# Performance work log

Hardware: AMD Instinct MI355X
Metric: run time of the kernel (lower is better)

Reference implementation:

```python
import jax, jax.numpy as jnp
import numpy as np

D_MODEL = 1024
NUM_HEADS = 16
HEAD_DIM = D_MODEL // NUM_HEADS


def setup_inputs() -> dict:
    key = jax.random.key(0)
    ks = jax.random.split(key, 9)
    B, S = 4, 2048
    s = 1.0 / np.sqrt(D_MODEL)
    return {
        "x": jax.random.normal(ks[0], (B, S, D_MODEL), dtype=jnp.float32),
        "Wq": jax.random.normal(ks[1], (D_MODEL, D_MODEL), dtype=jnp.float32) * s,
        "bq": jnp.zeros((D_MODEL,), dtype=jnp.float32),
        "Wk": jax.random.normal(ks[2], (D_MODEL, HEAD_DIM), dtype=jnp.float32) * s,
        "bk": jnp.zeros((HEAD_DIM,), dtype=jnp.float32),
        "Wv": jax.random.normal(ks[3], (D_MODEL, HEAD_DIM), dtype=jnp.float32) * s,
        "bv": jnp.zeros((HEAD_DIM,), dtype=jnp.float32),
        "Wo": jax.random.normal(ks[4], (D_MODEL, D_MODEL), dtype=jnp.float32) * s,
        "bo": jnp.zeros((D_MODEL,), dtype=jnp.float32),
    }


def reference(x, Wq, bq, Wk, bk, Wv, bv, Wo, bo):
    B, S, _ = x.shape
    H, Dh = NUM_HEADS, HEAD_DIM
    # projections
    Q = (x @ Wq + bq).reshape(B, S, H, Dh).transpose(0, 2, 1, 3)  # [B,H,S,Dh]
    K = x @ Wk + bk  # [B,S,Dh] (single shared KV head)
    V = x @ Wv + bv  # [B,S,Dh]
    # scores: Q @ K^T, broadcasting the single K head over all query heads
    A = jnp.einsum("bhqd,bkd->bhqk", Q, K)  # [B,H,S,S]
    causal = jnp.tril(jnp.ones((S, S), dtype=bool))
    A = jnp.where(causal, A, -jnp.inf)
    # original divides AFTER masking; -inf stays -inf so math is identical
    P = jax.nn.softmax(A / np.sqrt(Dh).astype(np.float32), axis=-1)
    O = jnp.einsum("bhqk,bkd->bhqd", P, V)  # [B,H,S,Dh]
    O = O.transpose(0, 2, 1, 3).reshape(B, S, H * Dh)
    return O @ Wo + bo
```

## Files before the change

### kernel.cpp

```cpp
#include <hip/hip_runtime.h>
#include <hip/hip_bf16.h>

typedef __bf16 bf16_t;
typedef __bf16 bf16x4 __attribute__((ext_vector_type(4)));
typedef __bf16 bf16x8 __attribute__((ext_vector_type(8)));
typedef float f32x4 __attribute__((ext_vector_type(4)));

#define AS1(p) ((const __attribute__((address_space(1))) void*)(p))
#define AS3(p) ((__attribute__((address_space(3))) void*)(p))

__device__ __forceinline__ f32x4 mfma16(bf16x8 a, bf16x8 b, f32x4 c) {
  return __builtin_amdgcn_mfma_f32_16x16x32_bf16(a, b, c, 0, 0, 0);
}

__global__ void prep(const float* __restrict__ x, const float* __restrict__ Wq,
                     const float* __restrict__ Wk, const float* __restrict__ Wv,
                     const float* __restrict__ Wo, const float* __restrict__ bk,
                     const float* __restrict__ bv, bf16_t* __restrict__ xb,
                     bf16_t* __restrict__ WqT, bf16_t* __restrict__ WkvT,
                     bf16_t* __restrict__ WoT, float* __restrict__ bkv) {
  const int u = blockIdx.x;
  if (u >= 545) {
    int i = ((u - 545) * 256 + threadIdx.x) * 4;
    float4 v = *(const float4*)(x + i);
    bf16x4 o = {(bf16_t)v.x, (bf16_t)v.y, (bf16_t)v.z, (bf16_t)v.w};
    *(bf16x4*)(xb + i) = o;
    return;
  }
  if (u == 544) {
    if (threadIdx.x < 128)
      bkv[threadIdx.x] = (threadIdx.x < 64) ? bk[threadIdx.x] : bv[threadIdx.x - 64];
    return;
  }
  const float* W; bf16_t* Wt; int N, bx, by;
  if (u < 256)      { W = Wq; Wt = WqT;             N = 1024; bx = u & 15;        by = u >> 4; }
  else if (u < 272) { W = Wk; Wt = WkvT;            N = 64;   bx = 0;             by = u - 256; }
  else if (u < 288) { W = Wv; Wt = WkvT + 64 * 1024; N = 64;  bx = 0;             by = u - 272; }
  else              { W = Wo; Wt = WoT;             N = 1024; bx = (u - 288) & 15; by = (u - 288) >> 4; }
  __shared__ float t[64][65];
  const int n0 = bx * 64, k0 = by * 64;
  const int tx = threadIdx.x & 63, ty = threadIdx.x >> 6;
#pragma unroll
  for (int i = 0; i < 16; ++i)
    t[ty * 16 + i][tx] = W[(size_t)(k0 + ty * 16 + i) * N + n0 + tx];
  __syncthreads();
#pragma unroll
  for (int i = 0; i < 16; ++i)
    Wt[(size_t)(n0 + ty * 16 + i) * 1024 + k0 + tx] = (bf16_t)t[tx][ty * 16 + i];
}

__global__ __launch_bounds__(256, 2)
void gemm_nt_bias_b16(const bf16_t* __restrict__ A, const bf16_t* __restrict__ Bt,
                      const float* __restrict__ bias, bf16_t* __restrict__ C,
                      int M, int N, int K) {
  __shared__ __align__(16) bf16_t As[128 * 32];
  __shared__ __align__(16) bf16_t Bs[128 * 32];
  const int tid = threadIdx.x;
  const int w = tid >> 6, l = tid & 63;
  const int l15 = l & 15, q = l >> 4;
  const int m0 = blockIdx.x * 128, n0 = blockIdx.y * 128;
  const int mw = (w >> 1) * 64, nw = (w & 1) * 64;
  f32x4 acc[4][4] = {};
  const int kb = (l & 3) * 8;
  int rA[2], rB[2];
#pragma unroll
  for (int i = 0; i < 2; ++i) {
    int row = (i * 4 + w) * 16 + (l >> 2);
    rA[i] = m0 + row;
    int rb = n0 + row; if (rb >= N) rb = N - 1;
    rB[i] = rb;
  }
  for (int k0 = 0; k0 < K; k0 += 32) {
#pragma unroll
    for (int i = 0; i < 2; ++i) {
      int sg = i * 4 + w;
      __builtin_amdgcn_global_load_lds(AS1(A + (size_t)rA[i] * K + k0 + kb),
                                       AS3(As + sg * 512), 16, 0, 0);
      __builtin_amdgcn_global_load_lds(AS1(Bt + (size_t)rB[i] * K + k0 + kb),
                                       AS3(Bs + sg * 512), 16, 0, 0);
    }
    __syncthreads();
    bf16x8 af[4], bfr[4];
#pragma unroll
    for (int mi = 0; mi < 4; ++mi)
      af[mi] = *(const bf16x8*)(As + (mw + mi * 16 + l15) * 32 + q * 8);
#pragma unroll
    for (int ni = 0; ni < 4; ++ni)
      bfr[ni] = *(const bf16x8*)(Bs + (nw + ni * 16 + l15) * 32 + q * 8);
#pragma unroll
    for (int mi = 0; mi < 4; ++mi)
#pragma unroll
      for (int ni = 0; ni < 4; ++ni)
        acc[mi][ni] = mfma16(af[mi], bfr[ni], acc[mi][ni]);
    __syncthreads();
  }
#pragma unroll
  for (int ni = 0; ni < 4; ++ni) {
    int col = n0 + nw + ni * 16 + l15;
    if (col >= N) continue;
    float bv = bias[col];
#pragma unroll
    for (int mi = 0; mi < 4; ++mi)
#pragma unroll
      for (int r = 0; r < 4; ++r) {
        int row = m0 + mw + mi * 16 + q * 4 + r;
        C[(size_t)row * N + col] = (bf16_t)(acc[mi][ni][r] + bv);
      }
  }
}

__global__ __launch_bounds__(256, 2)
void gemm_kv(const bf16_t* __restrict__ A, const bf16_t* __restrict__ Bt,
             const float* __restrict__ bias, bf16_t* __restrict__ C,
             bf16_t* __restrict__ VtG, int M, int K) {
  __shared__ __align__(16) bf16_t As[128 * 32];
  __shared__ __align__(16) bf16_t Bs[128 * 32];
  const int tid = threadIdx.x;
  const int w = tid >> 6, l = tid & 63;
  const int l15 = l & 15, q = l >> 4;
  const int m0 = blockIdx.x * 128;
  const int mw = (w >> 1) * 64, nw = (w & 1) * 64;
  f32x4 acc[4][4] = {};
  const int kb = (l & 3) * 8;
  int rA[2], rB[2];
#pragma unroll
  for (int i = 0; i < 2; ++i) {
    int row = (i * 4 + w) * 16 + (l >> 2);
    rA[i] = m0 + row;
    rB[i] = row;
  }
  for (int k0 = 0; k0 < K; k0 += 32) {
#pragma unroll
    for (int i = 0; i < 2; ++i) {
      int sg = i * 4 + w;
      __builtin_amdgcn_global_load_lds(AS1(A + (size_t)rA[i] * K + k0 + kb),
                                       AS3(As + sg * 512), 16, 0, 0);
      __builtin_amdgcn_global_load_lds(AS1(Bt + (size_t)rB[i] * K + k0 + kb),
                                       AS3(Bs + sg * 512), 16, 0, 0);
    }
    __syncthreads();
    bf16x8 af[4], bfr[4];
#pragma unroll
    for (int mi = 0; mi < 4; ++mi)
      af[mi] = *(const bf16x8*)(As + (mw + mi * 16 + l15) * 32 + q * 8);
#pragma unroll
    for (int ni = 0; ni < 4; ++ni)
      bfr[ni] = *(const bf16x8*)(Bs + (nw + ni * 16 + l15) * 32 + q * 8);
#pragma unroll
    for (int mi = 0; mi < 4; ++mi)
#pragma unroll
      for (int ni = 0; ni < 4; ++ni)
        acc[mi][ni] = mfma16(af[mi], bfr[ni], acc[mi][ni]);
    __syncthreads();
  }
#pragma unroll
  for (int ni = 0; ni < 4; ++ni) {
    int col = nw + ni * 16 + l15;
    float bv = bias[col];
#pragma unroll
    for (int mi = 0; mi < 4; ++mi)
#pragma unroll
      for (int r = 0; r < 4; ++r) {
        int row = m0 + mw + mi * 16 + q * 4 + r;
        bf16_t v = (bf16_t)(acc[mi][ni][r] + bv);
        C[(size_t)row * 128 + col] = v;
        if (col >= 64)
          VtG[(size_t)((row >> 11) * 64 + (col - 64)) * 2048 + (row & 2047)] = v;
      }
  }
}

__global__ __launch_bounds__(256, 2)
void gemm_nt_bias_f32(const bf16_t* __restrict__ A, const bf16_t* __restrict__ Bt,
                      const float* __restrict__ bias, float* __restrict__ C,
                      int M, int N, int K) {
  __shared__ __align__(16) bf16_t As[128 * 32];
  __shared__ __align__(16) bf16_t Bs[128 * 32];
  const int tid = threadIdx.x;
  const int w = tid >> 6, l = tid & 63;
  const int l15 = l & 15, q = l >> 4;
  const int m0 = blockIdx.x * 128, n0 = blockIdx.y * 128;
  const int mw = (w >> 1) * 64, nw = (w & 1) * 64;
  f32x4 acc[4][4] = {};
  const int kb = (l & 3) * 8;
  int rA[2], rB[2];
#pragma unroll
  for (int i = 0; i < 2; ++i) {
    int row = (i * 4 + w) * 16 + (l >> 2);
    rA[i] = m0 + row;
    int rb = n0 + row; if (rb >= N) rb = N - 1;
    rB[i] = rb;
  }
  for (int k0 = 0; k0 < K; k0 += 32) {
#pragma unroll
    for (int i = 0; i < 2; ++i) {
      int sg = i * 4 + w;
      __builtin_amdgcn_global_load_lds(AS1(A + (size_t)rA[i] * K + k0 + kb),
                                       AS3(As + sg * 512), 16, 0, 0);
      __builtin_amdgcn_global_load_lds(AS1(Bt + (size_t)rB[i] * K + k0 + kb),
                                       AS3(Bs + sg * 512), 16, 0, 0);
    }
    __syncthreads();
    bf16x8 af[4], bfr[4];
#pragma unroll
    for (int mi = 0; mi < 4; ++mi)
      af[mi] = *(const bf16x8*)(As + (mw + mi * 16 + l15) * 32 + q * 8);
#pragma unroll
    for (int ni = 0; ni < 4; ++ni)
      bfr[ni] = *(const bf16x8*)(Bs + (nw + ni * 16 + l15) * 32 + q * 8);
#pragma unroll
    for (int mi = 0; mi < 4; ++mi)
#pragma unroll
      for (int ni = 0; ni < 4; ++ni)
        acc[mi][ni] = mfma16(af[mi], bfr[ni], acc[mi][ni]);
    __syncthreads();
  }
#pragma unroll
  for (int ni = 0; ni < 4; ++ni) {
    int col = n0 + nw + ni * 16 + l15;
    if (col >= N) continue;
    float bv = bias[col];
#pragma unroll
    for (int mi = 0; mi < 4; ++mi)
#pragma unroll
      for (int r = 0; r < 4; ++r) {
        int row = m0 + mw + mi * 16 + q * 4 + r;
        C[(size_t)row * N + col] = acc[mi][ni][r] + bv;
      }
  }
}

__device__ __forceinline__ void load_q(const bf16_t* __restrict__ Qb, int b, int h,
                                       int qt, int l15, int q,
                                       bf16x8 (&qf0)[4], bf16x8 (&qf1)[4]) {
#pragma unroll
  for (int nq = 0; nq < 4; ++nq) {
    const bf16_t* qp = Qb + (size_t)(b * 2048 + qt * 64 + nq * 16 + l15) * 1024 + h * 64 + q * 8;
    qf0[nq] = *(const bf16x8*)qp;
    qf1[nq] = *(const bf16x8*)(qp + 32);
  }
}

template <bool DIAG>
__device__ __forceinline__ void attn_step(
    const bf16_t* __restrict__ kbase, const bf16_t* __restrict__ vbase, int kt,
    int l15, int q, bf16_t* __restrict__ ps,
    const bf16x8 (&qf0)[4], const bf16x8 (&qf1)[4],
    f32x4 (&o)[4][4], float (&rs)[4]) {
  const float c1 = 0.18033688f;
  const bf16_t* kb = kbase + (size_t)kt * 64 * 128;
  bf16x8 ka0[4], ka1[4];
#pragma unroll
  for (int mk = 0; mk < 4; ++mk) {
    const bf16_t* kr = kb + (mk * 16 + l15) * 128;
    ka0[mk] = *(const bf16x8*)(kr + q * 8);
    ka1[mk] = *(const bf16x8*)(kr + 32 + q * 8);
  }
  bf16x8 va0[4], va1[4];
#pragma unroll
  for (int md = 0; md < 4; ++md) {
    const bf16_t* vr = vbase + (size_t)(md * 16 + l15) * 2048 + kt * 64;
    va0[md] = *(const bf16x8*)(vr + q * 8);
    va1[md] = *(const bf16x8*)(vr + 32 + q * 8);
  }
#pragma unroll
  for (int mh = 0; mh < 2; ++mh) {
    f32x4 s2[2][4];
    __builtin_amdgcn_s_setprio(1);
#pragma unroll
    for (int mk2 = 0; mk2 < 2; ++mk2)
#pragma unroll
      for (int nq = 0; nq < 4; ++nq) {
        f32x4 t = {0.f, 0.f, 0.f, 0.f};
        t = mfma16(ka0[mh * 2 + mk2], qf0[nq], t);
        t = mfma16(ka1[mh * 2 + mk2], qf1[nq], t);
        s2[mk2][nq] = t;
      }
    __builtin_amdgcn_s_setprio(0);
#pragma unroll
    for (int nq = 0; nq < 4; ++nq)
#pragma unroll
      for (int mk2 = 0; mk2 < 2; ++mk2) {
        const int mk = mh * 2 + mk2;
        bf16x4 pk;
#pragma unroll
        for (int r = 0; r < 4; ++r) {
          float pv = __builtin_amdgcn_exp2f(s2[mk2][nq][r] * c1 - 16.0f);
          if (DIAG && (mk * 16 + q * 4 + r) > (nq * 16 + l15)) pv = 0.f;
          rs[nq] += pv;
          pk[r] = (bf16_t)pv;
        }
        *(bf16x4*)(ps + nq * 1152 + l15 * 72 + mk * 16 + q * 4) = pk;
      }
  }
#pragma unroll
  for (int nq = 0; nq < 4; ++nq) {
    bf16x8 pb0 = *(const bf16x8*)(ps + nq * 1152 + l15 * 72 + q * 8);
    bf16x8 pb1 = *(const bf16x8*)(ps + nq * 1152 + l15 * 72 + 32 + q * 8);
    __builtin_amdgcn_s_setprio(1);
#pragma unroll
    for (int md = 0; md < 4; ++md) {
      o[md][nq] = mfma16(va0[md], pb0, o[md][nq]);
      o[md][nq] = mfma16(va1[md], pb1, o[md][nq]);
    }
    __builtin_amdgcn_s_setprio(0);
  }
}

__device__ __forceinline__ void attn_finalize(bf16_t* __restrict__ AO, int b, int h,
                                              int qt, int l15, int q,
                                              f32x4 (&o)[4][4], float (&rs)[4]) {
#pragma unroll
  for (int nq = 0; nq < 4; ++nq) {
    rs[nq] += __shfl_xor(rs[nq], 16);
    rs[nq] += __shfl_xor(rs[nq], 32);
  }
  float inv[4];
#pragma unroll
  for (int nq = 0; nq < 4; ++nq) inv[nq] = 1.f / rs[nq];
#pragma unroll
  for (int md = 0; md < 4; ++md)
#pragma unroll
    for (int nq = 0; nq < 4; ++nq) {
      bf16x4 ov = {(bf16_t)(o[md][nq][0] * inv[nq]), (bf16_t)(o[md][nq][1] * inv[nq]),
                   (bf16_t)(o[md][nq][2] * inv[nq]), (bf16_t)(o[md][nq][3] * inv[nq])};
      *(bf16x4*)(AO + (size_t)(b * 2048 + qt * 64 + nq * 16 + l15) * 1024 +
                 h * 64 + md * 16 + q * 4) = ov;
    }
}

__global__ __launch_bounds__(128, 2)
void mqa_attn9(const bf16_t* __restrict__ Qb, const bf16_t* __restrict__ KVb,
               const bf16_t* __restrict__ VtG, bf16_t* __restrict__ AO) {
  __shared__ __align__(16) bf16_t Ps[2][4][16 * 72];
  __shared__ __align__(16) float Oc[4096];
  __shared__ float RSc[256];
  const int u = blockIdx.x;
  const int b = u & 3;
  const int h = (u >> 2) & 15;
  const int p = (u >> 6) & 15;
  const int w = threadIdx.x >> 6, l = threadIdx.x & 63;
  const int l15 = l & 15, q = l >> 4;
  const int qt_h = 31 - p;
  bf16_t* ps = &Ps[w][0][0];
  const bf16_t* kbase = KVb + (size_t)b * 2048 * 128;
  const bf16_t* vbase = VtG + (size_t)b * 64 * 2048;

  bf16x8 qf0[4], qf1[4];
  f32x4 o[4][4] = {};
  float rs[4] = {0.f, 0.f, 0.f, 0.f};

  if (w == 0) {
    load_q(Qb, b, h, qt_h, l15, q, qf0, qf1);
    const int e = (p == 15) ? 16 : 17;
    for (int kt = 0; kt < e; ++kt)
      attn_step<false>(kbase, vbase, kt, l15, q, ps, qf0, qf1, o, rs);
    if (p == 15)
      attn_step<true>(kbase, vbase, 16, l15, q, ps, qf0, qf1, o, rs);
    __syncthreads();
#pragma unroll
    for (int md = 0; md < 4; ++md)
#pragma unroll
      for (int nq = 0; nq < 4; ++nq)
        o[md][nq] += *(const f32x4*)&Oc[((md * 4 + nq) * 64 + l) * 4];
#pragma unroll
    for (int nq = 0; nq < 4; ++nq) rs[nq] += RSc[l * 4 + nq];
    attn_finalize(AO, b, h, qt_h, l15, q, o, rs);
  } else {
    load_q(Qb, b, h, p, l15, q, qf0, qf1);
    for (int kt = 0; kt < p; ++kt)
      attn_step<false>(kbase, vbase, kt, l15, q, ps, qf0, qf1, o, rs);
    attn_step<true>(kbase, vbase, p, l15, q, ps, qf0, qf1, o, rs);
    attn_finalize(AO, b, h, p, l15, q, o, rs);
#pragma unroll
    for (int md = 0; md < 4; ++md)
#pragma unroll
      for (int nq = 0; nq < 4; ++nq) o[md][nq] = f32x4{0.f, 0.f, 0.f, 0.f};
    rs[0] = rs[1] = rs[2] = rs[3] = 0.f;
    if (p < 15) {
      load_q(Qb, b, h, qt_h, l15, q, qf0, qf1);
      for (int kt = 17; kt < 31 - p; ++kt)
        attn_step<false>(kbase, vbase, kt, l15, q, ps, qf0, qf1, o, rs);
      attn_step<true>(kbase, vbase, 31 - p, l15, q, ps, qf0, qf1, o, rs);
    }
#pragma unroll
    for (int md = 0; md < 4; ++md)
#pragma unroll
      for (int nq = 0; nq < 4; ++nq)
        *(f32x4*)&Oc[((md * 4 + nq) * 64 + l) * 4] = o[md][nq];
#pragma unroll
    for (int nq = 0; nq < 4; ++nq) RSc[l * 4 + nq] = rs[nq];
    __syncthreads();
  }
}

extern "C" void kernel_launch(void* const* d_in, const int* in_sizes, int n_in,
                              void* d_out, int out_size, void* d_ws, size_t ws_size,
                              hipStream_t stream) {
  (void)in_sizes; (void)n_in; (void)out_size; (void)ws_size;
  const int BS = 8192;
  const float* x  = (const float*)d_in[0];
  const float* Wq = (const float*)d_in[1];
  const float* bq = (const float*)d_in[2];
  const float* Wk = (const float*)d_in[3];
  const float* bk = (const float*)d_in[4];
  const float* Wv = (const float*)d_in[5];
  const float* bv = (const float*)d_in[6];
  const float* Wo = (const float*)d_in[7];
  const float* bo = (const float*)d_in[8];
  float* out = (float*)d_out;

  bf16_t* p = (bf16_t*)d_ws;
  bf16_t* WqT  = p; p += 1024 * 1024;
  bf16_t* WkvT = p; p += 128 * 1024;
  bf16_t* WoT  = p; p += 1024 * 1024;
  bf16_t* xb   = p; p += (size_t)BS * 1024;
  bf16_t* Qb   = p; p += (size_t)BS * 1024;
  bf16_t* KVb  = p; p += (size_t)BS * 128;
  float*  bkv  = (float*)p; p += 256;
  bf16_t* AO  = xb;
  bf16_t* VtG = WqT;

  prep<<<dim3(545 + BS * 1024 / 1024), 256, 0, stream>>>(
      x, Wq, Wk, Wv, Wo, bk, bv, xb, WqT, WkvT, WoT, bkv);

  gemm_nt_bias_b16<<<dim3(BS / 128, 8), 256, 0, stream>>>(xb, WqT, bq, Qb, BS, 1024, 1024);
  gemm_kv<<<dim3(BS / 128, 1), 256, 0, stream>>>(xb, WkvT, bkv, KVb, VtG, BS, 1024);

  mqa_attn9<<<dim3(1024), 128, 0, stream>>>(Qb, KVb, VtG, AO);

  gemm_nt_bias_f32<<<dim3(BS / 128, 8), 256, 0, stream>>>(AO, WoT, bo, out, BS, 1024, 1024);
}
```

Before: 247.9 us.

## Fuse Q and KV projection GEMMs and double-buffer K tiles in attention

Merges the Q projection GEMM and the KV projection GEMM into one launch over a 9-column-tile grid. It relies on WqT and WkvT being contiguous in the workspace (1152 rows total), with the biases concatenated into one buffer. VtG now gets its own workspace region because WqT can no longer be overwritten. The attention kernel adds a software-pipelined loop that prefetches the next K tile and the current V tile into registers before computing each step. Together these aim to remove a launch and its tail inefficiency and to hide global load latency, at the cost of higher register pressure.

```diff
diff --git a/kernel.cpp b/kernel.cpp
--- a/kernel.cpp
+++ b/kernel.cpp
@@ -15,28 +15,35 @@
 
 __global__ void prep(const float* __restrict__ x, const float* __restrict__ Wq,
                      const float* __restrict__ Wk, const float* __restrict__ Wv,
-                     const float* __restrict__ Wo, const float* __restrict__ bk,
-                     const float* __restrict__ bv, bf16_t* __restrict__ xb,
-                     bf16_t* __restrict__ WqT, bf16_t* __restrict__ WkvT,
-                     bf16_t* __restrict__ WoT, float* __restrict__ bkv) {
+                     const float* __restrict__ Wo, const float* __restrict__ bq,
+                     const float* __restrict__ bk, const float* __restrict__ bv,
+                     bf16_t* __restrict__ xb, bf16_t* __restrict__ WqT,
+                     bf16_t* __restrict__ WkvT, bf16_t* __restrict__ WoT,
+                     float* __restrict__ bqkv) {
   const int u = blockIdx.x;
-  if (u >= 545) {
-    int i = ((u - 545) * 256 + threadIdx.x) * 4;
+  if (u >= 546) {
+    int i = ((u - 546) * 256 + threadIdx.x) * 4;
     float4 v = *(const float4*)(x + i);
     bf16x4 o = {(bf16_t)v.x, (bf16_t)v.y, (bf16_t)v.z, (bf16_t)v.w};
     *(bf16x4*)(xb + i) = o;
     return;
   }
   if (u == 544) {
+    int i = threadIdx.x * 4;
+    *(float4*)(bqkv + i) = *(const float4*)(bq + i);
+    return;
+  }
+  if (u == 545) {
     if (threadIdx.x < 128)
-      bkv[threadIdx.x] = (threadIdx.x < 64) ? bk[threadIdx.x] : bv[threadIdx.x - 64];
+      bqkv[1024 + threadIdx.x] =
+          (threadIdx.x < 64) ? bk[threadIdx.x] : bv[threadIdx.x - 64];
     return;
   }
   const float* W; bf16_t* Wt; int N, bx, by;
-  if (u < 256)      { W = Wq; Wt = WqT;             N = 1024; bx = u & 15;        by = u >> 4; }
-  else if (u < 272) { W = Wk; Wt = WkvT;            N = 64;   bx = 0;             by = u - 256; }
-  else if (u < 288) { W = Wv; Wt = WkvT + 64 * 1024; N = 64;  bx = 0;             by = u - 272; }
-  else              { W = Wo; Wt = WoT;             N = 1024; bx = (u - 288) & 15; by = (u - 288) >> 4; }
+  if (u < 256)      { W = Wq; Wt = WqT;              N = 1024; bx = u & 15;         by = u >> 4; }
+  else if (u < 272) { W = Wk; Wt = WkvT;             N = 64;   bx = 0;              by = u - 256; }
+  else if (u < 288) { W = Wv; Wt = WkvT + 64 * 1024; N = 64;   bx = 0;              by = u - 272; }
+  else              { W = Wo; Wt = WoT;              N = 1024; bx = (u - 288) & 15; by = (u - 288) >> 4; }
   __shared__ float t[64][65];
   const int n0 = bx * 64, k0 = by * 64;
   const int tx = threadIdx.x & 63, ty = threadIdx.x >> 6;
@@ -50,9 +57,9 @@
 }
 
 __global__ __launch_bounds__(256, 2)
-void gemm_nt_bias_b16(const bf16_t* __restrict__ A, const bf16_t* __restrict__ Bt,
-                      const float* __restrict__ bias, bf16_t* __restrict__ C,
-                      int M, int N, int K) {
+void gemm_qkv(const bf16_t* __restrict__ A, const bf16_t* __restrict__ Bt,
+              const float* __restrict__ bias, bf16_t* __restrict__ Qb,
+              bf16_t* __restrict__ KVb, bf16_t* __restrict__ VtG, int M, int K) {
   __shared__ __align__(16) bf16_t As[128 * 32];
   __shared__ __align__(16) bf16_t Bs[128 * 32];
   const int tid = threadIdx.x;
@@ -67,8 +74,7 @@
   for (int i = 0; i < 2; ++i) {
     int row = (i * 4 + w) * 16 + (l >> 2);
     rA[i] = m0 + row;
-    int rb = n0 + row; if (rb >= N) rb = N - 1;
-    rB[i] = rb;
+    rB[i] = n0 + row;
   }
   for (int k0 = 0; k0 < K; k0 += 32) {
 #pragma unroll
@@ -97,65 +103,6 @@
 #pragma unroll
   for (int ni = 0; ni < 4; ++ni) {
     int col = n0 + nw + ni * 16 + l15;
-    if (col >= N) continue;
-    float bv = bias[col];
-#pragma unroll
-    for (int mi = 0; mi < 4; ++mi)
-#pragma unroll
-      for (int r = 0; r < 4; ++r) {
-        int row = m0 + mw + mi * 16 + q * 4 + r;
-        C[(size_t)row * N + col] = (bf16_t)(acc[mi][ni][r] + bv);
-      }
-  }
-}
-
-__global__ __launch_bounds__(256, 2)
-void gemm_kv(const bf16_t* __restrict__ A, const bf16_t* __restrict__ Bt,
-             const float* __restrict__ bias, bf16_t* __restrict__ C,
-             bf16_t* __restrict__ VtG, int M, int K) {
-  __shared__ __align__(16) bf16_t As[128 * 32];
-  __shared__ __align__(16) bf16_t Bs[128 * 32];
-  const int tid = threadIdx.x;
-  const int w = tid >> 6, l = tid & 63;
-  const int l15 = l & 15, q = l >> 4;
-  const int m0 = blockIdx.x * 128;
-  const int mw = (w >> 1) * 64, nw = (w & 1) * 64;
-  f32x4 acc[4][4] = {};
-  const int kb = (l & 3) * 8;
-  int rA[2], rB[2];
-#pragma unroll
-  for (int i = 0; i < 2; ++i) {
-    int row = (i * 4 + w) * 16 + (l >> 2);
-    rA[i] = m0 + row;
-    rB[i] = row;
-  }
-  for (int k0 = 0; k0 < K; k0 += 32) {
-#pragma unroll
-    for (int i = 0; i < 2; ++i) {
-      int sg = i * 4 + w;
-      __builtin_amdgcn_global_load_lds(AS1(A + (size_t)rA[i] * K + k0 + kb),
-                                       AS3(As + sg * 512), 16, 0, 0);
-      __builtin_amdgcn_global_load_lds(AS1(Bt + (size_t)rB[i] * K + k0 + kb),
-                                       AS3(Bs + sg * 512), 16, 0, 0);
-    }
-    __syncthreads();
-    bf16x8 af[4], bfr[4];
-#pragma unroll
-    for (int mi = 0; mi < 4; ++mi)
-      af[mi] = *(const bf16x8*)(As + (mw + mi * 16 + l15) * 32 + q * 8);
-#pragma unroll
-    for (int ni = 0; ni < 4; ++ni)
-      bfr[ni] = *(const bf16x8*)(Bs + (nw + ni * 16 + l15) * 32 + q * 8);
-#pragma unroll
-    for (int mi = 0; mi < 4; ++mi)
-#pragma unroll
-      for (int ni = 0; ni < 4; ++ni)
-        acc[mi][ni] = mfma16(af[mi], bfr[ni], acc[mi][ni]);
-    __syncthreads();
-  }
-#pragma unroll
-  for (int ni = 0; ni < 4; ++ni) {
-    int col = nw + ni * 16 + l15;
     float bv = bias[col];
 #pragma unroll
     for (int mi = 0; mi < 4; ++mi)
@@ -163,9 +110,14 @@
       for (int r = 0; r < 4; ++r) {
         int row = m0 + mw + mi * 16 + q * 4 + r;
         bf16_t v = (bf16_t)(acc[mi][ni][r] + bv);
-        C[(size_t)row * 128 + col] = v;
-        if (col >= 64)
-          VtG[(size_t)((row >> 11) * 64 + (col - 64)) * 2048 + (row & 2047)] = v;
+        if (col < 1024) {
+          Qb[(size_t)row * 1024 + col] = v;
+        } else {
+          int c2 = col - 1024;
+          KVb[(size_t)row * 128 + c2] = v;
+          if (c2 >= 64)
+            VtG[(size_t)((row >> 11) * 64 + (c2 - 64)) * 2048 + (row & 2047)] = v;
+        }
       }
   }
 }
@@ -230,39 +182,35 @@
   }
 }
 
-__device__ __forceinline__ void load_q(const bf16_t* __restrict__ Qb, int b, int h,
-                                       int qt, int l15, int q,
-                                       bf16x8 (&qf0)[4], bf16x8 (&qf1)[4]) {
-#pragma unroll
-  for (int nq = 0; nq < 4; ++nq) {
-    const bf16_t* qp = Qb + (size_t)(b * 2048 + qt * 64 + nq * 16 + l15) * 1024 + h * 64 + q * 8;
-    qf0[nq] = *(const bf16x8*)qp;
-    qf1[nq] = *(const bf16x8*)(qp + 32);
+struct F8 { bf16x8 a0[4], a1[4]; };
+
+__device__ __forceinline__ void load_kf(F8& f, const bf16_t* __restrict__ kbase,
+                                        int kt, int l15, int q) {
+  const bf16_t* kb = kbase + (size_t)kt * 64 * 128;
+#pragma unroll
+  for (int mk = 0; mk < 4; ++mk) {
+    const bf16_t* kr = kb + (mk * 16 + l15) * 128;
+    f.a0[mk] = *(const bf16x8*)(kr + q * 8);
+    f.a1[mk] = *(const bf16x8*)(kr + 32 + q * 8);
+  }
+}
+
+__device__ __forceinline__ void load_vf(F8& f, const bf16_t* __restrict__ vbase,
+                                        int kt, int l15, int q) {
+#pragma unroll
+  for (int md = 0; md < 4; ++md) {
+    const bf16_t* vr = vbase + (size_t)(md * 16 + l15) * 2048 + kt * 64;
+    f.a0[md] = *(const bf16x8*)(vr + q * 8);
+    f.a1[md] = *(const bf16x8*)(vr + 32 + q * 8);
   }
 }
 
 template <bool DIAG>
 __device__ __forceinline__ void attn_step(
-    const bf16_t* __restrict__ kbase, const bf16_t* __restrict__ vbase, int kt,
-    int l15, int q, bf16_t* __restrict__ ps,
+    const F8& kf, const F8& vf, int l15, int q, bf16_t* __restrict__ ps,
     const bf16x8 (&qf0)[4], const bf16x8 (&qf1)[4],
     f32x4 (&o)[4][4], float (&rs)[4]) {
   const float c1 = 0.18033688f;
-  const bf16_t* kb = kbase + (size_t)kt * 64 * 128;
-  bf16x8 ka0[4], ka1[4];
-#pragma unroll
-  for (int mk = 0; mk < 4; ++mk) {
-    const bf16_t* kr = kb + (mk * 16 + l15) * 128;
-    ka0[mk] = *(const bf16x8*)(kr + q * 8);
-    ka1[mk] = *(const bf16x8*)(kr + 32 + q * 8);
-  }
-  bf16x8 va0[4], va1[4];
-#pragma unroll
-  for (int md = 0; md < 4; ++md) {
-    const bf16_t* vr = vbase + (size_t)(md * 16 + l15) * 2048 + kt * 64;
-    va0[md] = *(const bf16x8*)(vr + q * 8);
-    va1[md] = *(const bf16x8*)(vr + 32 + q * 8);
-  }
 #pragma unroll
   for (int mh = 0; mh < 2; ++mh) {
     f32x4 s2[2][4];
@@ -272,8 +220,8 @@
 #pragma unroll
       for (int nq = 0; nq < 4; ++nq) {
         f32x4 t = {0.f, 0.f, 0.f, 0.f};
-        t = mfma16(ka0[mh * 2 + mk2], qf0[nq], t);
-        t = mfma16(ka1[mh * 2 + mk2], qf1[nq], t);
+        t = mfma16(kf.a0[mh * 2 + mk2], qf0[nq], t);
+        t = mfma16(kf.a1[mh * 2 + mk2], qf1[nq], t);
         s2[mk2][nq] = t;
       }
     __builtin_amdgcn_s_setprio(0);
@@ -300,10 +248,64 @@
     __builtin_amdgcn_s_setprio(1);
 #pragma unroll
     for (int md = 0; md < 4; ++md) {
-      o[md][nq] = mfma16(va0[md], pb0, o[md][nq]);
-      o[md][nq] = mfma16(va1[md], pb1, o[md][nq]);
+      o[md][nq] = mfma16(vf.a0[md], pb0, o[md][nq]);
+      o[md][nq] = mfma16(vf.a1[md], pb1, o[md][nq]);
     }
     __builtin_amdgcn_s_setprio(0);
+  }
+}
+
+template <bool ENDDIAG>
+__device__ __forceinline__ void attn_run(
+    const bf16_t* __restrict__ kbase, const bf16_t* __restrict__ vbase,
+    int kt0, int ktN, int l15, int q, bf16_t* __restrict__ ps,
+    const bf16x8 (&qf0)[4], const bf16x8 (&qf1)[4],
+    f32x4 (&o)[4][4], float (&rs)[4]) {
+  F8 kA, kB, vf;
+  if (kt0 >= ktN) {
+    if (ENDDIAG) {
+      load_kf(kA, kbase, ktN, l15, q);
+      load_vf(vf, vbase, ktN, l15, q);
+      attn_step<true>(kA, vf, l15, q, ps, qf0, qf1, o, rs);
+    }
+    return;
+  }
+  load_kf(kA, kbase, kt0, l15, q);
+  int kt = kt0;
+  while (true) {
+    load_vf(vf, vbase, kt, l15, q);
+    if ((kt + 1 < ktN) || ENDDIAG) load_kf(kB, kbase, kt + 1, l15, q);
+    attn_step<false>(kA, vf, l15, q, ps, qf0, qf1, o, rs);
+    ++kt;
+    if (kt == ktN) {
+      if (ENDDIAG) {
+        load_vf(vf, vbase, kt, l15, q);
+        attn_step<true>(kB, vf, l15, q, ps, qf0, qf1, o, rs);
+      }
+      return;
+    }
+    load_vf(vf, vbase, kt, l15, q);
+    if ((kt + 1 < ktN) || ENDDIAG) load_kf(kA, kbase, kt + 1, l15, q);
+    attn_step<false>(kB, vf, l15, q, ps, qf0, qf1, o, rs);
+    ++kt;
+    if (kt == ktN) {
+      if (ENDDIAG) {
+        load_vf(vf, vbase, kt, l15, q);
+        attn_step<true>(kA, vf, l15, q, ps, qf0, qf1, o, rs);
+      }
+      return;
+    }
+  }
+}
+
+__device__ __forceinline__ void load_q(const bf16_t* __restrict__ Qb, int b, int h,
+                                       int qt, int l15, int q,
+                                       bf16x8 (&qf0)[4], bf16x8 (&qf1)[4]) {
+#pragma unroll
+  for (int nq = 0; nq < 4; ++nq) {
+    const bf16_t* qp = Qb + (size_t)(b * 2048 + qt * 64 + nq * 16 + l15) * 1024 + h * 64 + q * 8;
+    qf0[nq] = *(const bf16x8*)qp;
+    qf1[nq] = *(const bf16x8*)(qp + 32);
   }
 }
 
@@ -330,8 +332,8 @@
 }
 
 __global__ __launch_bounds__(128, 2)
-void mqa_attn9(const bf16_t* __restrict__ Qb, const bf16_t* __restrict__ KVb,
-               const bf16_t* __restrict__ VtG, bf16_t* __restrict__ AO) {
+void mqa_attn10(const bf16_t* __restrict__ Qb, const bf16_t* __restrict__ KVb,
+                const bf16_t* __restrict__ VtG, bf16_t* __restrict__ AO) {
   __shared__ __align__(16) bf16_t Ps[2][4][16 * 72];
   __shared__ __align__(16) float Oc[4096];
   __shared__ float RSc[256];
@@ -352,11 +354,10 @@
 
   if (w == 0) {
     load_q(Qb, b, h, qt_h, l15, q, qf0, qf1);
-    const int e = (p == 15) ? 16 : 17;
-    for (int kt = 0; kt < e; ++kt)
-      attn_step<false>(kbase, vbase, kt, l15, q, ps, qf0, qf1, o, rs);
     if (p == 15)
-      attn_step<true>(kbase, vbase, 16, l15, q, ps, qf0, qf1, o, rs);
+      attn_run<true>(kbase, vbase, 0, 16, l15, q, ps, qf0, qf1, o, rs);
+    else
+      attn_run<false>(kbase, vbase, 0, 17, l15, q, ps, qf0, qf1, o, rs);
     __syncthreads();
 #pragma unroll
     for (int md = 0; md < 4; ++md)
@@ -368,9 +369,7 @@
     attn_finalize(AO, b, h, qt_h, l15, q, o, rs);
   } else {
     load_q(Qb, b, h, p, l15, q, qf0, qf1);
-    for (int kt = 0; kt < p; ++kt)
-      attn_step<false>(kbase, vbase, kt, l15, q, ps, qf0, qf1, o, rs);
-    attn_step<true>(kbase, vbase, p, l15, q, ps, qf0, qf1, o, rs);
+    attn_run<true>(kbase, vbase, 0, p, l15, q, ps, qf0, qf1, o, rs);
     attn_finalize(AO, b, h, p, l15, q, o, rs);
 #pragma unroll
     for (int md = 0; md < 4; ++md)
@@ -379,9 +378,7 @@
     rs[0] = rs[1] = rs[2] = rs[3] = 0.f;
     if (p < 15) {
       load_q(Qb, b, h, qt_h, l15, q, qf0, qf1);
-      for (int kt = 17; kt < 31 - p; ++kt)
-        attn_step<false>(kbase, vbase, kt, l15, q, ps, qf0, qf1, o, rs);
-      attn_step<true>(kbase, vbase, 31 - p, l15, q, ps, qf0, qf1, o, rs);
+      attn_run<true>(kbase, vbase, 17, 31 - p, l15, q, ps, qf0, qf1, o, rs);
     }
 #pragma unroll
     for (int md = 0; md < 4; ++md)
@@ -417,17 +414,16 @@
   bf16_t* xb   = p; p += (size_t)BS * 1024;
   bf16_t* Qb   = p; p += (size_t)BS * 1024;
   bf16_t* KVb  = p; p += (size_t)BS * 128;
-  float*  bkv  = (float*)p; p += 256;
+  bf16_t* VtG  = p; p += (size_t)4 * 64 * 2048;
+  float*  bqkv = (float*)p; p += 2304;
   bf16_t* AO  = xb;
-  bf16_t* VtG = WqT;
-
-  prep<<<dim3(545 + BS * 1024 / 1024), 256, 0, stream>>>(
-      x, Wq, Wk, Wv, Wo, bk, bv, xb, WqT, WkvT, WoT, bkv);
-
-  gemm_nt_bias_b16<<<dim3(BS / 128, 8), 256, 0, stream>>>(xb, WqT, bq, Qb, BS, 1024, 1024);
-  gemm_kv<<<dim3(BS / 128, 1), 256, 0, stream>>>(xb, WkvT, bkv, KVb, VtG, BS, 1024);
-
-  mqa_attn9<<<dim3(1024), 128, 0, stream>>>(Qb, KVb, VtG, AO);
+
+  prep<<<dim3(546 + 8192), 256, 0, stream>>>(x, Wq, Wk, Wv, Wo, bq, bk, bv,
+                                             xb, WqT, WkvT, WoT, bqkv);
+
+  gemm_qkv<<<dim3(BS / 128, 9), 256, 0, stream>>>(xb, WqT, bqkv, Qb, KVb, VtG, BS, 1024);
+
+  mqa_attn10<<<dim3(1024), 128, 0, stream>>>(Qb, KVb, VtG, AO);
 
   gemm_nt_bias_f32<<<dim3(BS / 128, 8), 256, 0, stream>>>(AO, WoT, bo, out, BS, 1024, 1024);
 }
```

Result: slower. 272.1 us (+9.8%).
